# Kernel optimization log

Measured on AMD Instinct MI355X. Metric: run time of the kernel, lower is better.

## Reference

```python
import jax, jax.numpy as jnp
import numpy as np

B, N, G = 32, 1024, 8   # batch, Nvecs (= k_in), Nglobals
K_OUT, H = 128, 128     # MLP output width, hidden width
D_IN = 1 + N + G        # MLP input width: [u, norm, dots]


def setup_inputs() -> dict:
    key = jax.random.key(0)
    ks = jax.random.split(key, 8)
    x = jax.random.uniform(ks[0], (B, N, 3), dtype=jnp.float32)  # positive coords -> dots >= 0
    u = jax.random.normal(ks[1], (B, G), dtype=jnp.float32)
    s0 = 1.0 / np.sqrt(D_IN)
    s1 = 1.0 / np.sqrt(H)
    W0 = jax.random.normal(ks[2], (D_IN, H), dtype=jnp.float32) * s0
    b0 = jnp.zeros((H,), dtype=jnp.float32)
    W1 = jax.random.normal(ks[3], (H, H), dtype=jnp.float32) * s1
    b1 = jnp.zeros((H,), dtype=jnp.float32)
    W2 = jax.random.normal(ks[4], (H, K_OUT), dtype=jnp.float32) * s1
    b2 = jnp.zeros((K_OUT,), dtype=jnp.float32)
    return {"x": x, "u": u, "W0": W0, "b0": b0, "W1": W1, "b1": b1, "W2": W2, "b2": b2}


def reference(x, u, W0, b0, W1, b1, W2, b2):
    # x: [B, N, 3], u: [B, G]
    norms = jnp.linalg.norm(x, axis=-1, keepdims=True)            # [B, N, 1]
    dots = jnp.sqrt(jnp.einsum('bid,bjd->bij', x, x))             # [B, N, N]
    u_rep = jnp.broadcast_to(u[:, None, :], (x.shape[0], x.shape[1], u.shape[-1]))
    scalars = jnp.concatenate([u_rep, norms, dots], axis=-1)      # [B, N, G+1+N]
    # MLP (Linear -> LeakyReLU -> Linear -> LeakyReLU -> Linear)
    h = jax.nn.leaky_relu(scalars @ W0 + b0)
    h = jax.nn.leaky_relu(h @ W1 + b1)
    fk = h @ W2 + b2                                              # [B, N, K_OUT]
    # outer product 'bio,bid->biod' followed by mean over i == fused contraction
    out = jnp.einsum('bio,bid->bod', fk, x) / x.shape[1]          # [B, K_OUT, 3]
    return out
```

## Files before the change

kernel.cpp:

```cpp
#include <hip/hip_runtime.h>
#include <hip/hip_fp16.h>

typedef _Float16 f16;
typedef f16 f16x2 __attribute__((ext_vector_type(2)));
typedef f16 f16x8 __attribute__((ext_vector_type(8)));
typedef float f32x4 __attribute__((ext_vector_type(4)));

#define BB 32
#define NN 1024
#define HH 128

#define WT0_OFF   0
#define WT1_OFF   262144
#define WT2_OFF   294912
#define W8_OFF    327680
#define BIAS0_OFF 328192

__global__ __launch_bounds__(256) void prep_kernel(
    const float* __restrict__ u,  const float* __restrict__ W0,
    const float* __restrict__ b0, const float* __restrict__ W1,
    const float* __restrict__ W2,
    f16* __restrict__ Wt0, f16* __restrict__ Wt1, f16* __restrict__ Wt2,
    float* __restrict__ w8v, float* __restrict__ bias0)
{
    __shared__ __align__(16) f16 T[128 * 130];
    const int t = threadIdx.x;
    const int blk = blockIdx.x;
    if (blk < 16) {
        const int j0 = blk * 64;
        for (int k = 0; k < 32; ++k) {
            int flat = k * 256 + t;
            int j = flat >> 7, h = flat & 127;
            T[j * 130 + h] = (f16)W0[(9 + j0 + j) * 128 + h];
        }
        __syncthreads();
        for (int k = 0; k < 32; ++k) {
            int flat = k * 256 + t;
            int h = flat >> 6, jj = flat & 63;
            Wt0[h * 1024 + j0 + jj] = T[jj * 130 + h];
        }
    } else if (blk < 18) {
        const float* Ws = (blk == 16) ? W1 : W2;
        f16* Wd = (blk == 16) ? Wt1 : Wt2;
        for (int k = 0; k < 64; ++k) {
            int flat = k * 256 + t;
            int hi = flat >> 7, ho = flat & 127;
            T[ho * 130 + hi] = (f16)Ws[hi * 128 + ho];
        }
        __syncthreads();
        for (int k = 0; k < 64; ++k) {
            int flat = k * 256 + t;
            int ho = flat >> 7, hi = flat & 127;
            Wd[ho * 128 + hi] = T[ho * 130 + hi];
        }
    } else {
        if (t < 128) w8v[t] = W0[8 * 128 + t];
        for (int k = 0; k < 16; ++k) {
            int flat = k * 256 + t;
            int b = flat >> 7, h = flat & 127;
            float s = b0[h];
#pragma unroll
            for (int g = 0; g < 8; ++g) s += u[b * 8 + g] * W0[g * 128 + h];
            bias0[b * 128 + h] = s;
        }
    }
}

__global__ __launch_bounds__(256, 2) void fused_kernel(
    const float* __restrict__ x,   const float* __restrict__ b1p,
    const float* __restrict__ b2p,
    const f16* __restrict__ Wt0, const f16* __restrict__ Wt1,
    const f16* __restrict__ Wt2, const float* __restrict__ w8v,
    const float* __restrict__ bias0, float* __restrict__ outp)
{
    __shared__ __align__(16) f16 Dsh[64 * 136];
    __shared__ __align__(16) f16 Wsh[128 * 136];
    __shared__ __align__(16) f16 H0sh[64 * 136];
    __shared__ __align__(16) float xi[64 * 4];
    __shared__ __align__(16) float xj[128 * 4];
    __shared__ float normv[64];
    __shared__ float biass[128];
    __shared__ float w8s[128];

    const int t = threadIdx.x;
    const int bid = blockIdx.x;
    const int b = bid >> 4;
    const int i0 = (bid & 15) * 64;

    if (t < 192) {
        int i = t / 3, d = t - i * 3;
        xi[i * 4 + d] = x[((size_t)(b * NN + i0 + i)) * 3 + d];
    }
    if (t < 128) { biass[t] = bias0[b * 128 + t]; w8s[t] = w8v[t]; }
    __syncthreads();
    if (t < 64) {
        float a0 = xi[t * 4], a1 = xi[t * 4 + 1], a2 = xi[t * 4 + 2];
        normv[t] = __builtin_amdgcn_sqrtf(a0 * a0 + a1 * a1 + a2 * a2);
        xi[t * 4 + 3] = 0.f;
    }

    const int lane = t & 63, wv = t >> 6;
    const int wm = wv >> 1, wn = wv & 1;
    const int lm = lane & 15, q = lane >> 4;

    f32x4 acc[2][4];
#pragma unroll
    for (int mt = 0; mt < 2; ++mt)
#pragma unroll
        for (int nt = 0; nt < 4; ++nt)
#pragma unroll
            for (int e = 0; e < 4; ++e) acc[mt][nt][e] = 0.f;

    auto zero_acc = [&]() {
#pragma unroll
        for (int mt = 0; mt < 2; ++mt)
#pragma unroll
            for (int nt = 0; nt < 4; ++nt)
#pragma unroll
                for (int e = 0; e < 4; ++e) acc[mt][nt][e] = 0.f;
    };

    auto mfma_block = [&](const f16* Ab) {
#pragma unroll
        for (int ks = 0; ks < 4; ++ks) {
            const int ko = ks * 32 + q * 8;
            f16x8 af[2], bf[4];
#pragma unroll
            for (int mt = 0; mt < 2; ++mt)
                af[mt] = *(const f16x8*)(Ab + (wm * 32 + mt * 16 + lm) * 136 + ko);
#pragma unroll
            for (int nt = 0; nt < 4; ++nt)
                bf[nt] = *(const f16x8*)(Wsh + (wn * 64 + nt * 16 + lm) * 136 + ko);
#pragma unroll
            for (int mt = 0; mt < 2; ++mt)
#pragma unroll
                for (int nt = 0; nt < 4; ++nt)
                    acc[mt][nt] = __builtin_amdgcn_mfma_f32_16x16x32_f16(
                        af[mt], bf[nt], acc[mt][nt], 0, 0, 0);
        }
    };

    const int di = t >> 2;
    const int g4 = t & 3;

    for (int jc = 0; jc < 8; ++jc) {
        for (int idx = t; idx < 384; idx += 256) {
            int j = idx / 3, d = idx - j * 3;
            xj[j * 4 + d] = x[((size_t)(b * NN + jc * 128 + j)) * 3 + d];
        }
        {
            const int row = t >> 4, c8 = (t & 15) * 8;
#pragma unroll
            for (int r = 0; r < 8; ++r) {
                int rr = row + r * 16;
                *(uint4*)&Wsh[rr * 136 + c8] =
                    *(const uint4*)&Wt0[rr * 1024 + jc * 128 + c8];
            }
        }
        __syncthreads();
        {
            const float4 xiv = *(const float4*)&xi[di * 4];
#pragma unroll
            for (int tt = 0; tt < 16; ++tt) {
                int jo = ((tt + g4) & 15) * 2;
                int j = g4 * 32 + jo;
                float4 a = *(const float4*)&xj[j * 4];
                float4 c = *(const float4*)&xj[j * 4 + 4];
                float d0 = __builtin_amdgcn_sqrtf(
                    fmaf(xiv.x, a.x, fmaf(xiv.y, a.y, xiv.z * a.z)));
                float d1 = __builtin_amdgcn_sqrtf(
                    fmaf(xiv.x, c.x, fmaf(xiv.y, c.y, xiv.z * c.z)));
                f16x2 p; p.x = (f16)d0; p.y = (f16)d1;
                *(f16x2*)&Dsh[di * 136 + j] = p;
            }
        }
        __syncthreads();
        mfma_block(Dsh);
        __syncthreads();
    }

#pragma unroll
    for (int mt = 0; mt < 2; ++mt)
#pragma unroll
        for (int nt = 0; nt < 4; ++nt) {
            const int h = wn * 64 + nt * 16 + lm;
            const float bh = biass[h], w8h = w8s[h];
            f32x4 v = acc[mt][nt];
#pragma unroll
            for (int r = 0; r < 4; ++r) {
                int i = wm * 32 + mt * 16 + q * 4 + r;
                float val = v[r] + bh + normv[i] * w8h;
                val = val > 0.f ? val : 0.01f * val;
                H0sh[i * 136 + h] = (f16)val;
            }
        }
    {
        const int row = t >> 4, c8 = (t & 15) * 8;
#pragma unroll
        for (int r = 0; r < 8; ++r) {
            int rr = row + r * 16;
            *(uint4*)&Wsh[rr * 136 + c8] = *(const uint4*)&Wt1[rr * 128 + c8];
        }
    }
    __syncthreads();

    zero_acc();
    mfma_block(H0sh);
    __syncthreads();
#pragma unroll
    for (int mt = 0; mt < 2; ++mt)
#pragma unroll
        for (int nt = 0; nt < 4; ++nt) {
            const int h = wn * 64 + nt * 16 + lm;
            const float bh = b1p[h];
            f32x4 v = acc[mt][nt];
#pragma unroll
            for (int r = 0; r < 4; ++r) {
                int i = wm * 32 + mt * 16 + q * 4 + r;
                float val = v[r] + bh;
                val = val > 0.f ? val : 0.01f * val;
                Dsh[i * 136 + h] = (f16)val;
            }
        }
    {
        const int row = t >> 4, c8 = (t & 15) * 8;
#pragma unroll
        for (int r = 0; r < 8; ++r) {
            int rr = row + r * 16;
            *(uint4*)&Wsh[rr * 136 + c8] = *(const uint4*)&Wt2[rr * 128 + c8];
        }
    }
    __syncthreads();

    zero_acc();
    mfma_block(Dsh);

    float p[4][3];
#pragma unroll
    for (int nt = 0; nt < 4; ++nt)
#pragma unroll
        for (int d = 0; d < 3; ++d) p[nt][d] = 0.f;
    float bo[4];
#pragma unroll
    for (int nt = 0; nt < 4; ++nt) bo[nt] = b2p[wn * 64 + nt * 16 + lm];
#pragma unroll
    for (int mt = 0; mt < 2; ++mt)
#pragma unroll
        for (int r = 0; r < 4; ++r) {
            int i = wm * 32 + mt * 16 + q * 4 + r;
            float x0 = xi[i * 4], x1 = xi[i * 4 + 1], x2 = xi[i * 4 + 2];
#pragma unroll
            for (int nt = 0; nt < 4; ++nt) {
                float fkv = acc[mt][nt][r] + bo[nt];
                p[nt][0] = fmaf(fkv, x0, p[nt][0]);
                p[nt][1] = fmaf(fkv, x1, p[nt][1]);
                p[nt][2] = fmaf(fkv, x2, p[nt][2]);
            }
        }
#pragma unroll
    for (int nt = 0; nt < 4; ++nt)
#pragma unroll
        for (int d = 0; d < 3; ++d) {
            float s = p[nt][d];
            s += __shfl_xor(s, 16);
            s += __shfl_xor(s, 32);
            if (q == 0) {
                int o = wn * 64 + nt * 16 + lm;
                atomicAdd(&outp[(b * 128 + o) * 3 + d], s * (1.0f / 1024.0f));
            }
        }
}

extern "C" void kernel_launch(void* const* d_in, const int* in_sizes, int n_in,
                              void* d_out, int out_size, void* d_ws, size_t ws_size,
                              hipStream_t stream) {
    const float* x  = (const float*)d_in[0];
    const float* u  = (const float*)d_in[1];
    const float* W0 = (const float*)d_in[2];
    const float* b0 = (const float*)d_in[3];
    const float* W1 = (const float*)d_in[4];
    const float* b1 = (const float*)d_in[5];
    const float* W2 = (const float*)d_in[6];
    const float* b2 = (const float*)d_in[7];

    char* ws = (char*)d_ws;
    f16*   Wt0   = (f16*)(ws + WT0_OFF);
    f16*   Wt1   = (f16*)(ws + WT1_OFF);
    f16*   Wt2   = (f16*)(ws + WT2_OFF);
    float* w8v   = (float*)(ws + W8_OFF);
    float* bias0 = (float*)(ws + BIAS0_OFF);
    float* out   = (float*)d_out;

    hipMemsetAsync(d_out, 0, (size_t)out_size * sizeof(float), stream);
    prep_kernel<<<19, 256, 0, stream>>>(u, W0, b0, W1, W2, Wt0, Wt1, Wt2, w8v, bias0);
    fused_kernel<<<512, 256, 0, stream>>>(x, b1, b2, Wt0, Wt1, Wt2, w8v, bias0, out);
}
```

Measured before the change: 106.0 us.

## Double-buffer K-chunks, compute pairwise dots with MFMA, and swizzle LDS layout

The main loop now processes 64-wide K chunks with double-buffered LDS tiles. The next chunk's W0 slice is prefetched into registers and the next dot tile is computed while the current chunk's MFMAs run, which cuts the per-chunk barriers from two to one. The pairwise x·x dot products are now computed with a 16x16x16 f16 MFMA instead of scalar FMAs, so the coordinates are rounded to f16 before the dot rather than only after the sqrt. LDS tiles use an XOR swizzle instead of padding, which reduces shared memory and may raise occupancy, at the cost of extra address arithmetic and a small precision loss in the dots.

After: 100.4 us. -5.2%, faster.

```diff
diff --git a/kernel.cpp b/kernel.cpp
--- a/kernel.cpp
+++ b/kernel.cpp
@@ -2,13 +2,11 @@
 #include <hip/hip_fp16.h>
 
 typedef _Float16 f16;
-typedef f16 f16x2 __attribute__((ext_vector_type(2)));
+typedef f16 f16x4 __attribute__((ext_vector_type(4)));
 typedef f16 f16x8 __attribute__((ext_vector_type(8)));
 typedef float f32x4 __attribute__((ext_vector_type(4)));
 
-#define BB 32
 #define NN 1024
-#define HH 128
 
 #define WT0_OFF   0
 #define WT1_OFF   262144
@@ -73,23 +71,20 @@
     const f16* __restrict__ Wt2, const float* __restrict__ w8v,
     const float* __restrict__ bias0, float* __restrict__ outp)
 {
-    __shared__ __align__(16) f16 Dsh[64 * 136];
-    __shared__ __align__(16) f16 Wsh[128 * 136];
-    __shared__ __align__(16) f16 H0sh[64 * 136];
+    __shared__ __align__(16) f16 Dsh[2][64 * 64];
+    __shared__ __align__(16) f16 Wsh[2][128 * 64];
     __shared__ __align__(16) float xi[64 * 4];
-    __shared__ __align__(16) float xj[128 * 4];
     __shared__ float normv[64];
     __shared__ float biass[128];
     __shared__ float w8s[128];
 
     const int t = threadIdx.x;
-    const int bid = blockIdx.x;
-    const int b = bid >> 4;
-    const int i0 = (bid & 15) * 64;
+    const int b = blockIdx.x >> 4;
+    const int i0 = (blockIdx.x & 15) * 64;
 
     if (t < 192) {
         int i = t / 3, d = t - i * 3;
-        xi[i * 4 + d] = x[((size_t)(b * NN + i0 + i)) * 3 + d];
+        xi[i * 4 + d] = x[(size_t)(b * NN + i0 + i) * 3 + d];
     }
     if (t < 128) { biass[t] = bias0[b * 128 + t]; w8s[t] = w8v[t]; }
     __syncthreads();
@@ -98,19 +93,26 @@
         normv[t] = __builtin_amdgcn_sqrtf(a0 * a0 + a1 * a1 + a2 * a2);
         xi[t * 4 + 3] = 0.f;
     }
+    __syncthreads();
 
     const int lane = t & 63, wv = t >> 6;
     const int wm = wv >> 1, wn = wv & 1;
     const int lm = lane & 15, q = lane >> 4;
 
+    f16x4 bi[4];
+#pragma unroll
+    for (int it = 0; it < 4; ++it) {
+        f16x4 v; v[0] = (f16)0; v[1] = (f16)0; v[2] = (f16)0; v[3] = (f16)0;
+        if (q == 0) {
+            int ii = it * 16 + lm;
+            v[0] = (f16)xi[ii * 4];
+            v[1] = (f16)xi[ii * 4 + 1];
+            v[2] = (f16)xi[ii * 4 + 2];
+        }
+        bi[it] = v;
+    }
+
     f32x4 acc[2][4];
-#pragma unroll
-    for (int mt = 0; mt < 2; ++mt)
-#pragma unroll
-        for (int nt = 0; nt < 4; ++nt)
-#pragma unroll
-            for (int e = 0; e < 4; ++e) acc[mt][nt][e] = 0.f;
-
     auto zero_acc = [&]() {
 #pragma unroll
         for (int mt = 0; mt < 2; ++mt)
@@ -119,18 +121,52 @@
 #pragma unroll
                 for (int e = 0; e < 4; ++e) acc[mt][nt][e] = 0.f;
     };
-
-    auto mfma_block = [&](const f16* Ab) {
-#pragma unroll
-        for (int ks = 0; ks < 4; ++ks) {
-            const int ko = ks * 32 + q * 8;
+    zero_acc();
+
+    auto load_aj = [&](int jc) -> f16x4 {
+        f16x4 a; a[0] = (f16)0; a[1] = (f16)0; a[2] = (f16)0; a[3] = (f16)0;
+        if (q == 0) {
+            const float* p = x + (size_t)(b * NN + jc * 64 + wv * 16 + lm) * 3;
+            a[0] = (f16)p[0]; a[1] = (f16)p[1]; a[2] = (f16)p[2];
+        }
+        return a;
+    };
+
+    auto dotstore = [&](f16x4 aj, int buf) {
+        f32x4 cg[4];
+#pragma unroll
+        for (int it = 0; it < 4; ++it) {
+            f32x4 z; z[0] = 0.f; z[1] = 0.f; z[2] = 0.f; z[3] = 0.f;
+            cg[it] = __builtin_amdgcn_mfma_f32_16x16x16f16(aj, bi[it], z, 0, 0, 0);
+        }
+#pragma unroll
+        for (int it = 0; it < 4; ++it) {
+            f16x4 dv;
+#pragma unroll
+            for (int r = 0; r < 4; ++r)
+                dv[r] = (f16)__builtin_amdgcn_sqrtf(fmaxf(cg[it][r], 0.f));
+            int row = it * 16 + lm;
+            int colstart = wv * 16 + q * 4;
+            int addr = row * 64 + (((colstart & ~7) ^ ((row & 7) << 3)) | (colstart & 7));
+            *(f16x4*)&Dsh[buf][addr] = dv;
+        }
+    };
+
+    auto mfma2 = [&](const f16* Ab, const f16* Bb) {
+#pragma unroll
+        for (int ks = 0; ks < 2; ++ks) {
+            const int col = ks * 32 + q * 8;
             f16x8 af[2], bf[4];
 #pragma unroll
-            for (int mt = 0; mt < 2; ++mt)
-                af[mt] = *(const f16x8*)(Ab + (wm * 32 + mt * 16 + lm) * 136 + ko);
-#pragma unroll
-            for (int nt = 0; nt < 4; ++nt)
-                bf[nt] = *(const f16x8*)(Wsh + (wn * 64 + nt * 16 + lm) * 136 + ko);
+            for (int mt = 0; mt < 2; ++mt) {
+                int row = wm * 32 + mt * 16 + lm;
+                af[mt] = *(const f16x8*)(Ab + row * 64 + (col ^ ((row & 7) << 3)));
+            }
+#pragma unroll
+            for (int nt = 0; nt < 4; ++nt) {
+                int row = wn * 64 + nt * 16 + lm;
+                bf[nt] = *(const f16x8*)(Bb + row * 64 + (col ^ ((row & 7) << 3)));
+            }
 #pragma unroll
             for (int mt = 0; mt < 2; ++mt)
 #pragma unroll
@@ -140,43 +176,45 @@
         }
     };
 
-    const int di = t >> 2;
-    const int g4 = t & 3;
-
-    for (int jc = 0; jc < 8; ++jc) {
-        for (int idx = t; idx < 384; idx += 256) {
-            int j = idx / 3, d = idx - j * 3;
-            xj[j * 4 + d] = x[((size_t)(b * NN + jc * 128 + j)) * 3 + d];
-        }
-        {
-            const int row = t >> 4, c8 = (t & 15) * 8;
-#pragma unroll
-            for (int r = 0; r < 8; ++r) {
-                int rr = row + r * 16;
-                *(uint4*)&Wsh[rr * 136 + c8] =
-                    *(const uint4*)&Wt0[rr * 1024 + jc * 128 + c8];
-            }
-        }
+    auto stageW = [&](const f16* src, int stride, int srcCol, int buf) {
+#pragma unroll
+        for (int k = 0; k < 4; ++k) {
+            int uu = t + k * 256;
+            int row = uu >> 3, unit = uu & 7;
+            uint4 v = *(const uint4*)(src + row * stride + srcCol + unit * 8);
+            int addr = row * 64 + ((unit * 8) ^ ((row & 7) << 3));
+            *(uint4*)&Wsh[buf][addr] = v;
+        }
+    };
+
+    dotstore(load_aj(0), 0);
+    stageW(Wt0, 1024, 0, 0);
+    __syncthreads();
+
+    int cur = 0;
+    for (int jc = 0; jc < 16; ++jc) {
+        const int nxt = cur ^ 1;
+        const f16* wsrc = (jc < 15) ? Wt0 : Wt1;
+        const int wstride = (jc < 15) ? 1024 : 128;
+        const int wcol = (jc < 15) ? (jc + 1) * 64 : 0;
+        uint4 wreg[4];
+#pragma unroll
+        for (int k = 0; k < 4; ++k) {
+            int uu = t + k * 256;
+            int row = uu >> 3, unit = uu & 7;
+            wreg[k] = *(const uint4*)(wsrc + row * wstride + wcol + unit * 8);
+        }
+        if (jc < 15) dotstore(load_aj(jc + 1), nxt);
+#pragma unroll
+        for (int k = 0; k < 4; ++k) {
+            int uu = t + k * 256;
+            int row = uu >> 3, unit = uu & 7;
+            int addr = row * 64 + ((unit * 8) ^ ((row & 7) << 3));
+            *(uint4*)&Wsh[nxt][addr] = wreg[k];
+        }
+        mfma2(Dsh[cur], Wsh[cur]);
         __syncthreads();
-        {
-            const float4 xiv = *(const float4*)&xi[di * 4];
-#pragma unroll
-            for (int tt = 0; tt < 16; ++tt) {
-                int jo = ((tt + g4) & 15) * 2;
-                int j = g4 * 32 + jo;
-                float4 a = *(const float4*)&xj[j * 4];
-                float4 c = *(const float4*)&xj[j * 4 + 4];
-                float d0 = __builtin_amdgcn_sqrtf(
-                    fmaf(xiv.x, a.x, fmaf(xiv.y, a.y, xiv.z * a.z)));
-                float d1 = __builtin_amdgcn_sqrtf(
-                    fmaf(xiv.x, c.x, fmaf(xiv.y, c.y, xiv.z * c.z)));
-                f16x2 p; p.x = (f16)d0; p.y = (f16)d1;
-                *(f16x2*)&Dsh[di * 136 + j] = p;
-            }
-        }
-        __syncthreads();
-        mfma_block(Dsh);
-        __syncthreads();
+        cur = nxt;
     }
 
 #pragma unroll
@@ -185,55 +223,47 @@
         for (int nt = 0; nt < 4; ++nt) {
             const int h = wn * 64 + nt * 16 + lm;
             const float bh = biass[h], w8h = w8s[h];
-            f32x4 v = acc[mt][nt];
+            const int hh = h & 63;
 #pragma unroll
             for (int r = 0; r < 4; ++r) {
                 int i = wm * 32 + mt * 16 + q * 4 + r;
-                float val = v[r] + bh + normv[i] * w8h;
+                float val = acc[mt][nt][r] + bh + normv[i] * w8h;
                 val = val > 0.f ? val : 0.01f * val;
-                H0sh[i * 136 + h] = (f16)val;
-            }
-        }
-    {
-        const int row = t >> 4, c8 = (t & 15) * 8;
-#pragma unroll
-        for (int r = 0; r < 8; ++r) {
-            int rr = row + r * 16;
-            *(uint4*)&Wsh[rr * 136 + c8] = *(const uint4*)&Wt1[rr * 128 + c8];
-        }
-    }
+                int addr = i * 64 + (((hh & ~7) ^ ((i & 7) << 3)) | (hh & 7));
+                Dsh[wn][addr] = (f16)val;
+            }
+        }
+    stageW(Wt1, 128, 64, 1);
     __syncthreads();
 
     zero_acc();
-    mfma_block(H0sh);
-    __syncthreads();
+    mfma2(Dsh[0], Wsh[0]);
+    mfma2(Dsh[1], Wsh[1]);
+    __syncthreads();
+
 #pragma unroll
     for (int mt = 0; mt < 2; ++mt)
 #pragma unroll
         for (int nt = 0; nt < 4; ++nt) {
             const int h = wn * 64 + nt * 16 + lm;
             const float bh = b1p[h];
-            f32x4 v = acc[mt][nt];
+            const int hh = h & 63;
 #pragma unroll
             for (int r = 0; r < 4; ++r) {
                 int i = wm * 32 + mt * 16 + q * 4 + r;
-                float val = v[r] + bh;
+                float val = acc[mt][nt][r] + bh;
                 val = val > 0.f ? val : 0.01f * val;
-                Dsh[i * 136 + h] = (f16)val;
-            }
-        }
-    {
-        const int row = t >> 4, c8 = (t & 15) * 8;
-#pragma unroll
-        for (int r = 0; r < 8; ++r) {
-            int rr = row + r * 16;
-            *(uint4*)&Wsh[rr * 136 + c8] = *(const uint4*)&Wt2[rr * 128 + c8];
-        }
-    }
+                int addr = i * 64 + (((hh & ~7) ^ ((i & 7) << 3)) | (hh & 7));
+                Dsh[wn][addr] = (f16)val;
+            }
+        }
+    stageW(Wt2, 128, 0, 0);
+    stageW(Wt2, 128, 64, 1);
     __syncthreads();
 
     zero_acc();
-    mfma_block(Dsh);
+    mfma2(Dsh[0], Wsh[0]);
+    mfma2(Dsh[1], Wsh[1]);
 
     float p[4][3];
 #pragma unroll
```
